# Kernel tuning notes

Hardware: AMD Instinct MI355X
Metric: run time of the kernel (lower is better)

Reference implementation:

```python
import jax, jax.numpy as jnp
import numpy as np

N, E, D, D_OUT = 100000, 3200000, 64, 64
EPS = 1e-5


def setup_inputs() -> dict:
    key = jax.random.key(0)
    ks = jax.random.split(key, 16)
    s = 1.0 / np.sqrt(D)
    inp = {
        "x": jax.random.normal(ks[0], (N, D), dtype=jnp.float32),
        "edge_index": jax.random.randint(ks[1], (2, E), 0, N, dtype=jnp.int64),
        # layer 1: GCNConv weight/bias, fc weight/bias, BN gamma/beta
        "W1": jax.random.uniform(ks[2], (D, D), jnp.float32, -s, s),
        "b1": jnp.zeros((D,), jnp.float32),
        "fw1": jax.random.uniform(ks[3], (D, D), jnp.float32, -s, s),
        "fb1": jax.random.uniform(ks[4], (D,), jnp.float32, -s, s),
        "g1": jnp.ones((D,), jnp.float32),
        "bt1": jnp.zeros((D,), jnp.float32),
        # layer 2
        "W2": jax.random.uniform(ks[5], (D, D), jnp.float32, -s, s),
        "b2": jnp.zeros((D,), jnp.float32),
        "fw2": jax.random.uniform(ks[6], (D, D_OUT), jnp.float32, -s, s),
        "fb2": jax.random.uniform(ks[7], (D_OUT,), jnp.float32, -s, s),
        "g2": jnp.ones((D_OUT,), jnp.float32),
        "bt2": jnp.zeros((D_OUT,), jnp.float32),
    }
    return inp


def _gcn_conv(x, W, b, src, dst, dinv):
    # x' = X W, then symmetric-normalized scatter-add aggregation (self loops included)
    h = x @ W                                   # [N, D]
    msg = (dinv[src] * dinv[dst])[:, None] * h[src]  # [E+N, D]
    out = jax.ops.segment_sum(msg, dst, num_segments=N)
    return out + b


def _fc_bn_relu(x, fw, fb, g, bt):
    y = x @ fw + fb
    mu = jnp.mean(y, axis=0)
    var = jnp.mean((y - mu) ** 2, axis=0)  # biased var (torch BN training mode)
    y = (y - mu) * jax.lax.rsqrt(var + EPS) * g + bt
    return jax.nn.relu(y)


def reference(x, edge_index, W1, b1, fw1, fb1, g1, bt1, W2, b2, fw2, fb2, g2, bt2):
    loop = jnp.arange(N, dtype=edge_index.dtype)
    src = jnp.concatenate([edge_index[0], loop])  # add self loops
    dst = jnp.concatenate([edge_index[1], loop])
    deg = jax.ops.segment_sum(jnp.ones_like(dst, dtype=x.dtype), dst, num_segments=N)
    dinv = jax.lax.rsqrt(deg)  # deg >= 1 thanks to self loops

    h = _gcn_conv(x, W1, b1, src, dst, dinv)
    h = _fc_bn_relu(h, fw1, fb1, g1, bt1)
    h = _gcn_conv(h, W2, b2, src, dst, dinv)
    h = _fc_bn_relu(h, fw2, fb2, g2, bt2)
    return h
```

## Files before the change

kernel.cpp:

```cpp
#include <hip/hip_runtime.h>

#define N_NODES 100000
#define N_EDGES 3200000
#define D 64
#define EPS 1e-5f

#define BSHIFT 7
#define BNODES 128
#define NBUCK ((N_NODES + BNODES - 1) / BNODES)
#define P1_CHUNK 8192
#define NB_P1 ((N_EDGES + P1_CHUNK - 1) / P1_CHUNK)
#define SRC_MASK 0x1FFFFu
#define BCAP 4480
#define TBL_STRIDE 784

typedef __attribute__((ext_vector_type(8))) short bf16x8;
typedef __attribute__((ext_vector_type(4))) float f32x4;

__device__ __forceinline__ unsigned short f2bf(float f) {
  unsigned int u = __float_as_uint(f);
  u += 0x7FFFu + ((u >> 16) & 1u);
  return (unsigned short)(u >> 16);
}
__device__ __forceinline__ void addu4(float acc[8], uint4 u) {
  acc[0] += __uint_as_float(u.x << 16);
  acc[1] += __uint_as_float(u.x & 0xFFFF0000u);
  acc[2] += __uint_as_float(u.y << 16);
  acc[3] += __uint_as_float(u.y & 0xFFFF0000u);
  acc[4] += __uint_as_float(u.z << 16);
  acc[5] += __uint_as_float(u.z & 0xFFFF0000u);
  acc[6] += __uint_as_float(u.w << 16);
  acc[7] += __uint_as_float(u.w & 0xFFFF0000u);
}

__global__ __launch_bounds__(256) void combine_weights(
    const float* __restrict__ W1, const float* __restrict__ b1,
    const float* __restrict__ fw1, const float* __restrict__ fb1,
    const float* __restrict__ W2, const float* __restrict__ b2,
    const float* __restrict__ fw2, const float* __restrict__ fb2,
    unsigned int* __restrict__ WcB1, float* __restrict__ bc1,
    unsigned int* __restrict__ WcB2, float* __restrict__ bc2) {
  const float* W  = blockIdx.x ? W2  : W1;
  const float* fw = blockIdx.x ? fw2 : fw1;
  const float* b  = blockIdx.x ? b2  : b1;
  const float* fb = blockIdx.x ? fb2 : fb1;
  unsigned int* WcB = blockIdx.x ? WcB2 : WcB1;
  float* bc = blockIdx.x ? bc2 : bc1;

  __shared__ float sW[64 * 64];
  __shared__ float sf[64 * 64];
  __shared__ float sC[64 * 64];
  for (int i = threadIdx.x; i < 4096; i += 256) { sW[i] = W[i]; sf[i] = fw[i]; }
  __syncthreads();
  for (int o = threadIdx.x; o < 4096; o += 256) {
    int i = o >> 6, j = o & 63;
    float acc = 0.f;
    #pragma unroll
    for (int k = 0; k < 64; ++k) acc += sW[i * 64 + k] * sf[k * 64 + j];
    sC[o] = acc;
  }
  __syncthreads();
  for (int o = threadIdx.x; o < 2048; o += 256) {
    int jj = o & 3, L = (o >> 2) & 63, kh = (o >> 8) & 1, nt = o >> 9;
    int k0 = (L >> 4) * 8 + jj * 2 + kh * 32;
    int n  = nt * 16 + (L & 15);
    unsigned int lo = f2bf(sC[k0 * 64 + n]);
    unsigned int hi = f2bf(sC[(k0 + 1) * 64 + n]);
    WcB[o] = (hi << 16) | lo;
  }
  if (threadIdx.x < 64) {
    int j = threadIdx.x;
    float acc = fb[j];
    #pragma unroll
    for (int k = 0; k < 64; ++k) acc += b[k] * sf[k * 64 + j];
    bc[j] = acc;
  }
}

__global__ void zero_stats(float* __restrict__ stats) {
  if (threadIdx.x < 256) stats[threadIdx.x] = 0.0f;
}

__global__ __launch_bounds__(512) void pass1_sort(
    const int* __restrict__ src, const int* __restrict__ dst,
    unsigned int* __restrict__ stage, unsigned short* __restrict__ tbl) {
  __shared__ unsigned int hist[NBUCK];
  __shared__ unsigned int ts[512];
  __shared__ unsigned int sorted[P1_CHUNK];
  const int tid = threadIdx.x;
  const int e0 = blockIdx.x * P1_CHUNK;

  for (int b = tid; b < NBUCK; b += 512) hist[b] = 0;
  __syncthreads();

  int dreg[16];
  #pragma unroll
  for (int k = 0; k < 16; ++k) {
    int e = e0 + k * 512 + tid;
    int d = (e < N_EDGES) ? dst[e] : -1;
    dreg[k] = d;
    if (d >= 0) atomicAdd(&hist[((unsigned)d) >> BSHIFT], 1u);
  }
  __syncthreads();

  unsigned int v0 = (2 * tid < NBUCK) ? hist[2 * tid] : 0u;
  unsigned int v1 = (2 * tid + 1 < NBUCK) ? hist[2 * tid + 1] : 0u;
  unsigned int run = v0 + v1;
  ts[tid] = run;
  __syncthreads();
  for (int o = 1; o < 512; o <<= 1) {
    unsigned int add = (tid >= o) ? ts[tid - o] : 0u;
    __syncthreads();
    ts[tid] += add;
    __syncthreads();
  }
  const unsigned int excl = ts[tid] - run;
  const unsigned int m = ts[511];
  unsigned short* trow = tbl + (size_t)blockIdx.x * TBL_STRIDE;
  if (2 * tid < NBUCK)     { hist[2 * tid]     = excl;      trow[2 * tid]     = (unsigned short)excl; }
  if (2 * tid + 1 < NBUCK) { hist[2 * tid + 1] = excl + v0; trow[2 * tid + 1] = (unsigned short)(excl + v0); }
  if (tid == 0) trow[NBUCK] = (unsigned short)m;
  __syncthreads();

  #pragma unroll
  for (int k = 0; k < 16; ++k) {
    int e = e0 + k * 512 + tid;
    int t = dreg[k];
    if (t >= 0) {
      unsigned int pos = atomicAdd(&hist[((unsigned)t) >> BSHIFT], 1u);
      sorted[pos] = (((unsigned)(t & (BNODES - 1))) << 17) | (unsigned)src[e];
    }
  }
  __syncthreads();

  unsigned int* so = stage + (size_t)blockIdx.x * P1_CHUNK;
  for (int i = tid; i < (int)m; i += 512) so[i] = sorted[i];
}

__global__ __launch_bounds__(512) void pass2_sort(
    const unsigned int* __restrict__ stage, const unsigned short* __restrict__ tbl,
    int* __restrict__ eSrc, int* __restrict__ off, int* __restrict__ edeg,
    float* __restrict__ dinv) {
  __shared__ int segbase[NB_P1];
  __shared__ int spre[512];
  __shared__ int cnt[BNODES];
  __shared__ int ts[BNODES];
  __shared__ unsigned int raw[BCAP];
  __shared__ int sorted[BCAP];
  const int b = blockIdx.x, tid = threadIdx.x;
  const int n0 = b * BNODES;

  int len = 0;
  if (tid < NB_P1) {
    const unsigned short* trow = tbl + (size_t)tid * TBL_STRIDE;
    int o0 = trow[b], o1 = trow[b + 1];
    segbase[tid] = tid * P1_CHUNK + o0;
    len = o1 - o0;
  }
  if (tid < BNODES) cnt[tid] = 0;
  spre[tid] = len;
  __syncthreads();
  for (int o = 1; o < 512; o <<= 1) {
    int add = (tid >= o) ? spre[tid - o] : 0;
    __syncthreads();
    spre[tid] += add;
    __syncthreads();
  }
  const int m = spre[511];
  const int pref = spre[tid] - len;

  if (tid < NB_P1) {
    const int base = segbase[tid];
    for (int j = 0; j < len; ++j) {
      unsigned int p = stage[base + j];
      raw[pref + j] = p;
      atomicAdd(&cnt[p >> 17], 1);
    }
  }
  __syncthreads();

  int v = 0;
  if (tid < BNODES) { v = cnt[tid]; ts[tid] = v; }
  __syncthreads();
  for (int o = 1; o < BNODES; o <<= 1) {
    int add = (tid >= o && tid < BNODES) ? ts[tid - o] : 0;
    __syncthreads();
    if (tid < BNODES) ts[tid] += add;
    __syncthreads();
  }
  if (tid < BNODES) {
    int excl = ts[tid] - v;
    int node = n0 + tid;
    if (node < N_NODES) {
      off[node]  = b * BCAP + excl;
      edeg[node] = v;
      dinv[node] = rsqrtf((float)v + 1.0f);
    }
    cnt[tid] = excl;
  }
  __syncthreads();

  for (int i = tid; i < m; i += 512) {
    unsigned int p = raw[i];
    int pos = atomicAdd(&cnt[p >> 17], 1);
    if (pos < BCAP) sorted[pos] = (int)(p & SRC_MASK);
  }
  __syncthreads();

  int* out = eSrc + (size_t)b * BCAP;
  for (int i = tid; i < m; i += 512) out[i] = sorted[i];
}

__global__ void prescale_x(const float* __restrict__ x, const float* __restrict__ dinv,
                           unsigned short* __restrict__ Xs) {
  int idx = blockIdx.x * blockDim.x + threadIdx.x;
  if (idx < N_NODES * D) Xs[idx] = f2bf(dinv[idx >> 6] * x[idx]);
}

__global__ void prescale_y(const float* __restrict__ Y, const float* __restrict__ dinv,
                           const float* __restrict__ a, const float* __restrict__ c,
                           unsigned short* __restrict__ Ys) {
  int idx = blockIdx.x * blockDim.x + threadIdx.x;
  if (idx < N_NODES * D) {
    int i = idx >> 6, j = idx & 63;
    Ys[idx] = f2bf(dinv[i] * fmaxf(fmaf(Y[idx], a[j], c[j]), 0.f));
  }
}

__global__ __launch_bounds__(256) void agg_csr(
    const int* __restrict__ off, const int* __restrict__ edeg,
    const int* __restrict__ eSrc, const unsigned short* __restrict__ Xs,
    const float* __restrict__ dinv, unsigned short* __restrict__ agg) {
  const int wid = (blockIdx.x * 256 + threadIdx.x) >> 6;
  const int lane = threadIdx.x & 63;
  const int grp = lane >> 3, sub = lane & 7;
  if (wid >= N_NODES) return;
  const int s0 = off[wid];
  const int s1 = s0 + edeg[wid];
  const uint4* XsV = (const uint4*)Xs;

  float acc[8];
  {
    uint4 u = XsV[(size_t)wid * 8 + sub];
    if (grp != 0) { u.x = 0; u.y = 0; u.z = 0; u.w = 0; }
    acc[0] = __uint_as_float(u.x << 16);
    acc[1] = __uint_as_float(u.x & 0xFFFF0000u);
    acc[2] = __uint_as_float(u.y << 16);
    acc[3] = __uint_as_float(u.y & 0xFFFF0000u);
    acc[4] = __uint_as_float(u.z << 16);
    acc[5] = __uint_as_float(u.z & 0xFFFF0000u);
    acc[6] = __uint_as_float(u.w << 16);
    acc[7] = __uint_as_float(u.w & 0xFFFF0000u);
  }

  const int lim = s1 - 1;
  for (int e = s0; e < s1; e += 32) {
    int ea = e + grp, eb = e + 8 + grp, ec = e + 16 + grp, ed = e + 24 + grp;
    int sa = eSrc[min(ea, lim)];
    int sb = eSrc[min(eb, lim)];
    int sc = eSrc[min(ec, lim)];
    int sd = eSrc[min(ed, lim)];
    uint4 ua = XsV[(size_t)sa * 8 + sub];
    uint4 ub = XsV[(size_t)sb * 8 + sub];
    uint4 uc = XsV[(size_t)sc * 8 + sub];
    uint4 ud = XsV[(size_t)sd * 8 + sub];
    if (ea > lim) { ua.x = 0; ua.y = 0; ua.z = 0; ua.w = 0; }
    if (eb > lim) { ub.x = 0; ub.y = 0; ub.z = 0; ub.w = 0; }
    if (ec > lim) { uc.x = 0; uc.y = 0; uc.z = 0; uc.w = 0; }
    if (ed > lim) { ud.x = 0; ud.y = 0; ud.z = 0; ud.w = 0; }
    addu4(acc, ua); addu4(acc, ub); addu4(acc, uc); addu4(acc, ud);
  }

  #pragma unroll
  for (int mk = 8; mk <= 32; mk <<= 1) {
    #pragma unroll
    for (int i = 0; i < 8; ++i) acc[i] += __shfl_xor(acc[i], mk, 64);
  }

  if (grp == 0) {
    float dt = dinv[wid];
    uint4 o;
    o.x = ((unsigned)f2bf(acc[1] * dt) << 16) | f2bf(acc[0] * dt);
    o.y = ((unsigned)f2bf(acc[3] * dt) << 16) | f2bf(acc[2] * dt);
    o.z = ((unsigned)f2bf(acc[5] * dt) << 16) | f2bf(acc[4] * dt);
    o.w = ((unsigned)f2bf(acc[7] * dt) << 16) | f2bf(acc[6] * dt);
    *(uint4*)(agg + (size_t)wid * 64 + sub * 8) = o;
  }
}

__global__ __launch_bounds__(256) void gemm_stats(
    const unsigned short* __restrict__ A, const unsigned int* __restrict__ WcB,
    const float* __restrict__ bc, float* __restrict__ Y,
    float* __restrict__ colsum, float* __restrict__ colsq) {
  const int tid = threadIdx.x;
  const int L = tid & 63, wv = tid >> 6;
  const int quad = L >> 4, l16 = L & 15;

  const bf16x8* Wv = (const bf16x8*)WcB;
  bf16x8 bfr[4][2];
  #pragma unroll
  for (int nt = 0; nt < 4; ++nt)
    #pragma unroll
    for (int kh = 0; kh < 2; ++kh)
      bfr[nt][kh] = Wv[(nt * 2 + kh) * 64 + L];
  float bcv[4];
  #pragma unroll
  for (int nt = 0; nt < 4; ++nt) bcv[nt] = bc[nt * 16 + l16];

  const bf16x8* Av = (const bf16x8*)A;
  float psum[4] = {0.f, 0.f, 0.f, 0.f}, psq[4] = {0.f, 0.f, 0.f, 0.f};

  #pragma unroll
  for (int loop = 0; loop < 2; ++loop) {
    const int rowbase = blockIdx.x * 128 + loop * 64 + wv * 16;
    const int m = min(rowbase + l16, N_NODES - 1);
    bf16x8 a0 = Av[(size_t)m * 8 + quad];
    bf16x8 a1 = Av[(size_t)m * 8 + 4 + quad];
    #pragma unroll
    for (int nt = 0; nt < 4; ++nt) {
      f32x4 acc = {0.f, 0.f, 0.f, 0.f};
      acc = __builtin_amdgcn_mfma_f32_16x16x32_bf16(a0, bfr[nt][0], acc, 0, 0, 0);
      acc = __builtin_amdgcn_mfma_f32_16x16x32_bf16(a1, bfr[nt][1], acc, 0, 0, 0);
      #pragma unroll
      for (int r = 0; r < 4; ++r) {
        int row = rowbase + quad * 4 + r;
        if (row < N_NODES) {
          float y = acc[r] + bcv[nt];
          Y[(size_t)row * 64 + nt * 16 + l16] = y;
          psum[nt] += y;
          psq[nt] += y * y;
        }
      }
    }
  }

  #pragma unroll
  for (int nt = 0; nt < 4; ++nt) {
    psum[nt] += __shfl_xor(psum[nt], 16, 64);
    psum[nt] += __shfl_xor(psum[nt], 32, 64);
    psq[nt]  += __shfl_xor(psq[nt], 16, 64);
    psq[nt]  += __shfl_xor(psq[nt], 32, 64);
  }
  __shared__ float rsum[4][64];
  __shared__ float rsq[4][64];
  if (L < 16) {
    #pragma unroll
    for (int nt = 0; nt < 4; ++nt) {
      rsum[wv][nt * 16 + L] = psum[nt];
      rsq[wv][nt * 16 + L]  = psq[nt];
    }
  }
  __syncthreads();
  if (tid < 64) {
    float s = rsum[0][tid] + rsum[1][tid] + rsum[2][tid] + rsum[3][tid];
    float q = rsq[0][tid] + rsq[1][tid] + rsq[2][tid] + rsq[3][tid];
    atomicAdd(&colsum[tid], s);
    atomicAdd(&colsq[tid], q);
  }
}

__global__ void finalize_stats(const float* __restrict__ colsum, const float* __restrict__ colsq,
                               const float* __restrict__ g, const float* __restrict__ bt,
                               float* __restrict__ a, float* __restrict__ c) {
  int j = threadIdx.x;
  if (j < 64) {
    float mu = colsum[j] * (1.0f / N_NODES);
    float var = colsq[j] * (1.0f / N_NODES) - mu * mu;
    float s = rsqrtf(var + EPS) * g[j];
    a[j] = s;
    c[j] = bt[j] - mu * s;
  }
}

__global__ void final_norm(float* __restrict__ Y, const float* __restrict__ a,
                           const float* __restrict__ c) {
  int idx = blockIdx.x * blockDim.x + threadIdx.x;
  if (idx < N_NODES * D) {
    int j = idx & 63;
    Y[idx] = fmaxf(fmaf(Y[idx], a[j], c[j]), 0.f);
  }
}

extern "C" void kernel_launch(void* const* d_in, const int* in_sizes, int n_in,
                              void* d_out, int out_size, void* d_ws, size_t ws_size,
                              hipStream_t stream) {
  const float* x   = (const float*)d_in[0];
  const int*   src = (const int*)d_in[1];
  const int*   dst = src + N_EDGES;
  const float* W1  = (const float*)d_in[2];
  const float* b1  = (const float*)d_in[3];
  const float* fw1 = (const float*)d_in[4];
  const float* fb1 = (const float*)d_in[5];
  const float* g1  = (const float*)d_in[6];
  const float* bt1 = (const float*)d_in[7];
  const float* W2  = (const float*)d_in[8];
  const float* b2  = (const float*)d_in[9];
  const float* fw2 = (const float*)d_in[10];
  const float* fb2 = (const float*)d_in[11];
  const float* g2  = (const float*)d_in[12];
  const float* bt2 = (const float*)d_in[13];

  float* Y = (float*)d_out;

  unsigned char* w = (unsigned char*)d_ws;
  unsigned int*   stage = (unsigned int*)w;
  unsigned short* aggb  = (unsigned short*)w;
  size_t ofs = ((size_t)NB_P1 * P1_CHUNK * 4 + 255) & ~(size_t)255;
  float*          dinv  = (float*)(w + ofs);
  unsigned short* Xs    = (unsigned short*)(dinv + N_NODES);
  int*            eSrc  = (int*)(Xs + (size_t)N_NODES * D);
  int*            off   = eSrc + (size_t)NBUCK * BCAP;
  int*            edeg  = off + N_NODES;
  unsigned short* tbl   = (unsigned short*)(edeg + N_NODES);
  unsigned int* WcB1 = (unsigned int*)(tbl + (size_t)NB_P1 * TBL_STRIDE);
  float* bc1  = (float*)(WcB1 + 2048);
  unsigned int* WcB2 = (unsigned int*)(bc1 + 64);
  float* bc2  = (float*)(WcB2 + 2048);
  float* sum1 = bc2 + 64;
  float* sq1  = sum1 + 64;
  float* sum2 = sq1 + 64;
  float* sq2  = sum2 + 64;
  float* a1   = sq2 + 64;
  float* c1   = a1 + 64;
  float* a2   = c1 + 64;
  float* c2   = a2 + 64;

  const int nd = N_NODES * D;
  dim3 blk(256);

  combine_weights<<<2, blk, 0, stream>>>(W1, b1, fw1, fb1, W2, b2, fw2, fb2,
                                         WcB1, bc1, WcB2, bc2);
  zero_stats<<<1, blk, 0, stream>>>(sum1);

  pass1_sort<<<NB_P1, 512, 0, stream>>>(src, dst, stage, tbl);
  pass2_sort<<<NBUCK, 512, 0, stream>>>(stage, tbl, eSrc, off, edeg, dinv);

  prescale_x<<<(nd + 255) / 256, blk, 0, stream>>>(x, dinv, Xs);
  agg_csr<<<(nd + 255) / 256, blk, 0, stream>>>(off, edeg, eSrc, Xs, dinv, aggb);
  gemm_stats<<<(N_NODES + 127) / 128, blk, 0, stream>>>(aggb, WcB1, bc1, Y, sum1, sq1);
  finalize_stats<<<1, 64, 0, stream>>>(sum1, sq1, g1, bt1, a1, c1);

  prescale_y<<<(nd + 255) / 256, blk, 0, stream>>>(Y, dinv, a1, c1, Xs);
  agg_csr<<<(nd + 255) / 256, blk, 0, stream>>>(off, edeg, eSrc, Xs, dinv, aggb);
  gemm_stats<<<(N_NODES + 127) / 128, blk, 0, stream>>>(aggb, WcB2, bc2, Y, sum2, sq2);
  finalize_stats<<<1, 64, 0, stream>>>(sum2, sq2, g2, bt2, a2, c2);

  final_norm<<<(nd + 255) / 256, blk, 0, stream>>>(Y, a2, c2);
}
```

Baseline: 364.1 us.

## Fuse prescale into sort, store GEMM output as bf16, fold stats finalize into consumers

Folds stats zeroing into combine_weights, fuses prescale_x into pass2_sort using shared dinv, and folds finalize_stats into prescale_y and final_norm. gemm_stats now writes a bf16 intermediate into the reused Xs buffer rather than fp32 Y, which halves that traffic. agg_csr gains an unguarded main loop over full 32-edge chunks and float2 accumulators. Together these cut kernel launches and intermediate memory traffic, at the cost of extra bf16 rounding on the pre-BN activations.

```diff
diff --git a/kernel.cpp b/kernel.cpp
--- a/kernel.cpp
+++ b/kernel.cpp
@@ -22,15 +22,17 @@
   u += 0x7FFFu + ((u >> 16) & 1u);
   return (unsigned short)(u >> 16);
 }
-__device__ __forceinline__ void addu4(float acc[8], uint4 u) {
-  acc[0] += __uint_as_float(u.x << 16);
-  acc[1] += __uint_as_float(u.x & 0xFFFF0000u);
-  acc[2] += __uint_as_float(u.y << 16);
-  acc[3] += __uint_as_float(u.y & 0xFFFF0000u);
-  acc[4] += __uint_as_float(u.z << 16);
-  acc[5] += __uint_as_float(u.z & 0xFFFF0000u);
-  acc[6] += __uint_as_float(u.w << 16);
-  acc[7] += __uint_as_float(u.w & 0xFFFF0000u);
+__device__ __forceinline__ float bf2f(unsigned short h) {
+  return __uint_as_float(((unsigned int)h) << 16);
+}
+__device__ __forceinline__ float2 bfpair(unsigned int u) {
+  return make_float2(__uint_as_float(u << 16), __uint_as_float(u & 0xFFFF0000u));
+}
+__device__ __forceinline__ void addp(float2 a[4], uint4 u) {
+  a[0] += bfpair(u.x);
+  a[1] += bfpair(u.y);
+  a[2] += bfpair(u.z);
+  a[3] += bfpair(u.w);
 }
 
 __global__ __launch_bounds__(256) void combine_weights(
@@ -39,7 +41,12 @@
     const float* __restrict__ W2, const float* __restrict__ b2,
     const float* __restrict__ fw2, const float* __restrict__ fb2,
     unsigned int* __restrict__ WcB1, float* __restrict__ bc1,
-    unsigned int* __restrict__ WcB2, float* __restrict__ bc2) {
+    unsigned int* __restrict__ WcB2, float* __restrict__ bc2,
+    float* __restrict__ stats) {
+  if (blockIdx.x == 2) {
+    if (threadIdx.x < 256) stats[threadIdx.x] = 0.0f;
+    return;
+  }
   const float* W  = blockIdx.x ? W2  : W1;
   const float* fw = blockIdx.x ? fw2 : fw1;
   const float* b  = blockIdx.x ? b2  : b1;
@@ -75,10 +82,6 @@
     for (int k = 0; k < 64; ++k) acc += b[k] * sf[k * 64 + j];
     bc[j] = acc;
   }
-}
-
-__global__ void zero_stats(float* __restrict__ stats) {
-  if (threadIdx.x < 256) stats[threadIdx.x] = 0.0f;
 }
 
 __global__ __launch_bounds__(512) void pass1_sort(
@@ -140,11 +143,13 @@
 __global__ __launch_bounds__(512) void pass2_sort(
     const unsigned int* __restrict__ stage, const unsigned short* __restrict__ tbl,
     int* __restrict__ eSrc, int* __restrict__ off, int* __restrict__ edeg,
-    float* __restrict__ dinv) {
+    float* __restrict__ dinv, const float* __restrict__ x,
+    unsigned short* __restrict__ Xs) {
   __shared__ int segbase[NB_P1];
   __shared__ int spre[512];
   __shared__ int cnt[BNODES];
   __shared__ int ts[BNODES];
+  __shared__ float dinvL[BNODES];
   __shared__ unsigned int raw[BCAP];
   __shared__ int sorted[BCAP];
   const int b = blockIdx.x, tid = threadIdx.x;
@@ -191,10 +196,12 @@
   if (tid < BNODES) {
     int excl = ts[tid] - v;
     int node = n0 + tid;
+    float dv = rsqrtf((float)v + 1.0f);
+    dinvL[tid] = dv;
     if (node < N_NODES) {
       off[node]  = b * BCAP + excl;
       edeg[node] = v;
-      dinv[node] = rsqrtf((float)v + 1.0f);
+      dinv[node] = dv;
     }
     cnt[tid] = excl;
   }
@@ -209,21 +216,12 @@
 
   int* out = eSrc + (size_t)b * BCAP;
   for (int i = tid; i < m; i += 512) out[i] = sorted[i];
-}
-
-__global__ void prescale_x(const float* __restrict__ x, const float* __restrict__ dinv,
-                           unsigned short* __restrict__ Xs) {
-  int idx = blockIdx.x * blockDim.x + threadIdx.x;
-  if (idx < N_NODES * D) Xs[idx] = f2bf(dinv[idx >> 6] * x[idx]);
-}
-
-__global__ void prescale_y(const float* __restrict__ Y, const float* __restrict__ dinv,
-                           const float* __restrict__ a, const float* __restrict__ c,
-                           unsigned short* __restrict__ Ys) {
-  int idx = blockIdx.x * blockDim.x + threadIdx.x;
-  if (idx < N_NODES * D) {
-    int i = idx >> 6, j = idx & 63;
-    Ys[idx] = f2bf(dinv[i] * fmaxf(fmaf(Y[idx], a[j], c[j]), 0.f));
+
+  const int rows = min(BNODES, N_NODES - n0);
+  for (int i = tid; i < rows * 64; i += 512) {
+    int r = i >> 6;
+    size_t g = (size_t)(n0 + r) * 64 + (i & 63);
+    Xs[g] = f2bf(dinvL[r] * x[g]);
   }
 }
 
@@ -239,22 +237,31 @@
   const int s1 = s0 + edeg[wid];
   const uint4* XsV = (const uint4*)Xs;
 
-  float acc[8];
+  float2 acc[4];
   {
     uint4 u = XsV[(size_t)wid * 8 + sub];
     if (grp != 0) { u.x = 0; u.y = 0; u.z = 0; u.w = 0; }
-    acc[0] = __uint_as_float(u.x << 16);
-    acc[1] = __uint_as_float(u.x & 0xFFFF0000u);
-    acc[2] = __uint_as_float(u.y << 16);
-    acc[3] = __uint_as_float(u.y & 0xFFFF0000u);
-    acc[4] = __uint_as_float(u.z << 16);
-    acc[5] = __uint_as_float(u.z & 0xFFFF0000u);
-    acc[6] = __uint_as_float(u.w << 16);
-    acc[7] = __uint_as_float(u.w & 0xFFFF0000u);
-  }
-
-  const int lim = s1 - 1;
-  for (int e = s0; e < s1; e += 32) {
+    acc[0] = bfpair(u.x);
+    acc[1] = bfpair(u.y);
+    acc[2] = bfpair(u.z);
+    acc[3] = bfpair(u.w);
+  }
+
+  int e = s0;
+  const int eend = s1 - ((s1 - s0) & 31);
+  for (; e < eend; e += 32) {
+    int sa = eSrc[e + grp];
+    int sb = eSrc[e + 8 + grp];
+    int sc = eSrc[e + 16 + grp];
+    int sd = eSrc[e + 24 + grp];
+    uint4 ua = XsV[(size_t)sa * 8 + sub];
+    uint4 ub = XsV[(size_t)sb * 8 + sub];
+    uint4 uc = XsV[(size_t)sc * 8 + sub];
+    uint4 ud = XsV[(size_t)sd * 8 + sub];
+    addp(acc, ua); addp(acc, ub); addp(acc, uc); addp(acc, ud);
+  }
+  if (e < s1) {
+    const int lim = s1 - 1;
     int ea = e + grp, eb = e + 8 + grp, ec = e + 16 + grp, ed = e + 24 + grp;
     int sa = eSrc[min(ea, lim)];
     int sb = eSrc[min(eb, lim)];
@@ -268,29 +275,32 @@
     if (eb > lim) { ub.x = 0; ub.y = 0; ub.z = 0; ub.w = 0; }
     if (ec > lim) { uc.x = 0; uc.y = 0; uc.z = 0; uc.w = 0; }
     if (ed > lim) { ud.x = 0; ud.y = 0; ud.z = 0; ud.w = 0; }
-    addu4(acc, ua); addu4(acc, ub); addu4(acc, uc); addu4(acc, ud);
+    addp(acc, ua); addp(acc, ub); addp(acc, uc); addp(acc, ud);
   }
 
   #pragma unroll
   for (int mk = 8; mk <= 32; mk <<= 1) {
     #pragma unroll
-    for (int i = 0; i < 8; ++i) acc[i] += __shfl_xor(acc[i], mk, 64);
+    for (int i = 0; i < 4; ++i) {
+      acc[i].x += __shfl_xor(acc[i].x, mk, 64);
+      acc[i].y += __shfl_xor(acc[i].y, mk, 64);
+    }
   }
 
   if (grp == 0) {
     float dt = dinv[wid];
     uint4 o;
-    o.x = ((unsigned)f2bf(acc[1] * dt) << 16) | f2bf(acc[0] * dt);
-    o.y = ((unsigned)f2bf(acc[3] * dt) << 16) | f2bf(acc[2] * dt);
-    o.z = ((unsigned)f2bf(acc[5] * dt) << 16) | f2bf(acc[4] * dt);
-    o.w = ((unsigned)f2bf(acc[7] * dt) << 16) | f2bf(acc[6] * dt);
+    o.x = ((unsigned)f2bf(acc[0].y * dt) << 16) | f2bf(acc[0].x * dt);
+    o.y = ((unsigned)f2bf(acc[1].y * dt) << 16) | f2bf(acc[1].x * dt);
+    o.z = ((unsigned)f2bf(acc[2].y * dt) << 16) | f2bf(acc[2].x * dt);
+    o.w = ((unsigned)f2bf(acc[3].y * dt) << 16) | f2bf(acc[3].x * dt);
     *(uint4*)(agg + (size_t)wid * 64 + sub * 8) = o;
   }
 }
 
 __global__ __launch_bounds__(256) void gemm_stats(
     const unsigned short* __restrict__ A, const unsigned int* __restrict__ WcB,
-    const float* __restrict__ bc, float* __restrict__ Y,
+    const float* __restrict__ bc, unsigned short* __restrict__ Yb,
     float* __restrict__ colsum, float* __restrict__ colsq) {
   const int tid = threadIdx.x;
   const int L = tid & 63, wv = tid >> 6;
@@ -326,7 +336,7 @@
         int row = rowbase + quad * 4 + r;
         if (row < N_NODES) {
           float y = acc[r] + bcv[nt];
-          Y[(size_t)row * 64 + nt * 16 + l16] = y;
+          Yb[(size_t)row * 64 + nt * 16 + l16] = f2bf(y);
           psum[nt] += y;
           psq[nt] += y * y;
         }
@@ -359,25 +369,46 @@
   }
 }
 
-__global__ void finalize_stats(const float* __restrict__ colsum, const float* __restrict__ colsq,
-                               const float* __restrict__ g, const float* __restrict__ bt,
-                               float* __restrict__ a, float* __restrict__ c) {
-  int j = threadIdx.x;
-  if (j < 64) {
+__global__ __launch_bounds__(256) void prescale_y(
+    unsigned short* __restrict__ YbXs, const float* __restrict__ dinv,
+    const float* __restrict__ colsum, const float* __restrict__ colsq,
+    const float* __restrict__ g, const float* __restrict__ bt) {
+  __shared__ float sa[64], sc[64];
+  if (threadIdx.x < 64) {
+    int j = threadIdx.x;
     float mu = colsum[j] * (1.0f / N_NODES);
     float var = colsq[j] * (1.0f / N_NODES) - mu * mu;
     float s = rsqrtf(var + EPS) * g[j];
-    a[j] = s;
-    c[j] = bt[j] - mu * s;
-  }
-}
-
-__global__ void final_norm(float* __restrict__ Y, const float* __restrict__ a,
-                           const float* __restrict__ c) {
+    sa[j] = s;
+    sc[j] = bt[j] - mu * s;
+  }
+  __syncthreads();
+  int idx = blockIdx.x * blockDim.x + threadIdx.x;
+  if (idx < N_NODES * D) {
+    int i = idx >> 6, j = idx & 63;
+    float y = bf2f(YbXs[idx]);
+    YbXs[idx] = f2bf(dinv[i] * fmaxf(fmaf(y, sa[j], sc[j]), 0.f));
+  }
+}
+
+__global__ __launch_bounds__(256) void final_norm(
+    const unsigned short* __restrict__ Yb, float* __restrict__ out,
+    const float* __restrict__ colsum, const float* __restrict__ colsq,
+    const float* __restrict__ g, const float* __restrict__ bt) {
+  __shared__ float sa[64], sc[64];
+  if (threadIdx.x < 64) {
+    int j = threadIdx.x;
+    float mu = colsum[j] * (1.0f / N_NODES);
+    float var = colsq[j] * (1.0f / N_NODES) - mu * mu;
+    float s = rsqrtf(var + EPS) * g[j];
+    sa[j] = s;
+    sc[j] = bt[j] - mu * s;
+  }
+  __syncthreads();
   int idx = blockIdx.x * blockDim.x + threadIdx.x;
   if (idx < N_NODES * D) {
     int j = idx & 63;
-    Y[idx] = fmaxf(fmaf(Y[idx], a[j], c[j]), 0.f);
+    out[idx] = fmaxf(fmaf(bf2f(Yb[idx]), sa[j], sc[j]), 0.f);
   }
 }
 
@@ -400,15 +431,15 @@
   const float* g2  = (const float*)d_in[12];
   const float* bt2 = (const float*)d_in[13];
 
-  float* Y = (float*)d_out;
+  float* out = (float*)d_out;
 
   unsigned char* w = (unsigned char*)d_ws;
   unsigned int*   stage = (unsigned int*)w;
   unsigned short* aggb  = (unsigned short*)w;
   size_t ofs = ((size_t)NB_P1 * P1_CHUNK * 4 + 255) & ~(size_t)255;
   float*          dinv  = (float*)(w + ofs);
-  unsigned short* Xs    = (unsigned short*)(dinv + N_NODES);
-  int*            eSrc  = (int*)(Xs + (size_t)N_NODES * D);
+  unsigned short* XsYb  = (unsigned short*)(dinv + N_NODES);
+  int*            eSrc  = (int*)(XsYb + (size_t)N_NODES * D);
   int*            off   = eSrc + (size_t)NBUCK * BCAP;
   int*            edeg  = off + N_NODES;
   unsigned short* tbl   = (unsigned short*)(edeg + N_NODES);
@@ -420,30 +451,22 @@
   float* sq1  = sum1 + 64;
   float* sum2 = sq1 + 64;
   float* sq2  = sum2 + 64;
-  float* a1   = sq2 + 64;
-  float* c1   = a1 + 64;
-  float* a2   = c1 + 64;
-  float* c2   = a2 + 64;
 
   const int nd = N_NODES * D;
   dim3 blk(256);
 
-  combine_weights<<<2, blk, 0, stream>>>(W1, b1, fw1, fb1, W2, b2, fw2, fb2,
-                                         WcB1, bc1, WcB2, bc2);
-  zero_stats<<<1, blk, 0, stream>>>(sum1);
+  combine_weights<<<3, blk, 0, stream>>>(W1, b1, fw1, fb1, W2, b2, fw2, fb2,
+                                         WcB1, bc1, WcB2, bc2, sum1);
 
   pass1_sort<<<NB_P1, 512, 0, stream>>>(src, dst, stage, tbl);
-  pass2_sort<<<NBUCK, 512, 0, stream>>>(stage, tbl, eSrc, off, edeg, dinv);
-
-  prescale_x<<<(nd + 255) / 256, blk, 0, stream>>>(x, dinv, Xs);
-  agg_csr<<<(nd + 255) / 256, blk, 0, stream>>>(off, edeg, eSrc, Xs, dinv, aggb);
-  gemm_stats<<<(N_NODES + 127) / 128, blk, 0, stream>>>(aggb, WcB1, bc1, Y, sum1, sq1);
-  finalize_stats<<<1, 64, 0, stream>>>(sum1, sq1, g1, bt1, a1, c1);
-
-  prescale_y<<<(nd + 255) / 256, blk, 0, stream>>>(Y, dinv, a1, c1, Xs);
-  agg_csr<<<(nd + 255) / 256, blk, 0, stream>>>(off, edeg, eSrc, Xs, dinv, aggb);
-  gemm_stats<<<(N_NODES + 127) / 128, blk, 0, stream>>>(aggb, WcB2, bc2, Y, sum2, sq2);
-  finalize_stats<<<1, 64, 0, stream>>>(sum2, sq2, g2, bt2, a2, c2);
-
-  final_norm<<<(nd + 255) / 256, blk, 0, stream>>>(Y, a2, c2);
-}
+  pass2_sort<<<NBUCK, 512, 0, stream>>>(stage, tbl, eSrc, off, edeg, dinv, x, XsYb);
+
+  agg_csr<<<(nd + 255) / 256, blk, 0, stream>>>(off, edeg, eSrc, XsYb, dinv, aggb);
+  gemm_stats<<<(N_NODES + 127) / 128, blk, 0, stream>>>(aggb, WcB1, bc1, XsYb, sum1, sq1);
+
+  prescale_y<<<(nd + 255) / 256, blk, 0, stream>>>(XsYb, dinv, sum1, sq1, g1, bt1);
+  agg_csr<<<(nd + 255) / 256, blk, 0, stream>>>(off, edeg, eSrc, XsYb, dinv, aggb);
+  gemm_stats<<<(N_NODES + 127) / 128, blk, 0, stream>>>(aggb, WcB2, bc2, XsYb, sum2, sq2);
+
+  final_norm<<<(nd + 255) / 256, blk, 0, stream>>>(XsYb, out, sum2, sq2, g2, bt2);
+}
```

Measured after the change: 354.6 us. -2.6%, faster.
